# Kernel tuning notes

Hardware: AMD Instinct MI355X
Metric: run time of the kernel (lower is better)

The kernel has to match this reference:

```python
import jax, jax.numpy as jnp
import numpy as np
from itertools import permutations

N_NODES, B, C, H, W = 3, 4, 256, 40, 40
NO_PASS = 2


def _conv3x3(x, w, b):
    # x: [NB, Cin, H, W], w: [Cout, Cin, 3, 3]
    y = jax.lax.conv_general_dilated(
        x, w, window_strides=(1, 1), padding='SAME',
        dimension_numbers=('NCHW', 'OIHW', 'NCHW'))
    return y + b[None, :, None, None]


def setup_inputs() -> dict:
    key = jax.random.key(0)
    ks = jax.random.split(key, 7)
    s = 0.02
    return {
        'nodes': jax.random.normal(ks[0], (N_NODES, B, C, H, W), jnp.float32),
        'theta_w': jax.random.normal(ks[1], (C, C), jnp.float32) * s,
        'theta_b': jax.random.normal(ks[2], (C,), jnp.float32) * s,
        'gru_gates_w': jax.random.normal(ks[3], (2 * C, 2 * C, 3, 3), jnp.float32) * s,
        'gru_gates_b': jax.random.normal(ks[4], (2 * C,), jnp.float32) * s,
        'gru_can_w': jax.random.normal(ks[5], (C, 2 * C, 3, 3), jnp.float32) * s,
        'gru_can_b': jax.random.normal(ks[6], (C,), jnp.float32) * s,
    }


def reference(nodes, theta_w, theta_b, gru_gates_w, gru_gates_b, gru_can_w, gru_can_b):
    N, Bn, Cn, Hn, Wn = nodes.shape
    P = Hn * Wn
    edges = np.array(list(permutations(range(N), 2)))  # [E, 2]
    recv = jnp.asarray(edges[:, 0])  # edge[0] receives message
    send = jnp.asarray(edges[:, 1])  # edge[1] sends

    for _ in range(NO_PASS):
        nf = nodes.reshape(N, Bn, Cn, P)
        # theta is a 1x1 conv == channel matmul
        th = jnp.einsum('oc,nbcp->nbop', theta_w, nf) + theta_b[None, None, :, None]
        thi = th[recv]          # [E, B, C, P]
        ei = nf[recv]           # [E, B, C, P]
        ej = nf[send]           # [E, B, C, P]
        # scores[e,b,p,q] = theta(e1)[:,p] . e2[:,q]
        scores = jnp.einsum('ebcp,ebcq->ebpq', thi, ej)
        atn = jax.nn.softmax(scores, axis=-1)
        # message = atn @ (e2 + e1)^T, back to channel-first
        msg = jnp.einsum('ebpq,ebcq->ebcp', atn, ej + ei)  # [E, B, C, P]
        agg = jax.ops.segment_sum(msg, recv, num_segments=N)  # sum of incoming msgs

        # ConvGRU update, nodes folded into batch dim
        x = agg.reshape(N * Bn, Cn, Hn, Wn)
        h = nodes.reshape(N * Bn, Cn, Hn, Wn)
        gates = _conv3x3(jnp.concatenate([x, h], axis=1), gru_gates_w, gru_gates_b)
        r, z = jnp.split(jax.nn.sigmoid(gates), 2, axis=1)
        cand = jnp.tanh(_conv3x3(jnp.concatenate([x, r * h], axis=1), gru_can_w, gru_can_b))
        h_new = (1.0 - z) * h + z * cand
        nodes = h_new.reshape(N, Bn, Cn, Hn, Wn)
    return nodes
```

## Files before the change

### kernel.cpp

```cpp
#include <hip/hip_runtime.h>
#include <hip/hip_bf16.h>
#include <math.h>

#define NN 3
#define BB 4
#define CC 256
#define C2 512
#define HH 40
#define WW 40
#define PP 1600
#define NBB 12
#define NODESZ (NBB*CC*PP)
#define TO 16
#define PAD 1764

typedef short short8 __attribute__((ext_vector_type(8)));
typedef float f32x4 __attribute__((ext_vector_type(4)));
typedef unsigned short ushort_t;
typedef unsigned int uint_t;

__device__ __forceinline__ ushort_t f2bf(float x) {
  union { float f; uint_t u; } v; v.f = x;
  uint_t r = v.u + 0x7fff + ((v.u >> 16) & 1);
  return (ushort_t)(r >> 16);
}

__device__ __forceinline__ void async_ld16(const ushort_t* g, ushort_t* l) {
  __builtin_amdgcn_global_load_lds(
      (const __attribute__((address_space(1))) uint_t*)g,
      (__attribute__((address_space(3))) uint_t*)l, 16, 0, 0);
}

__global__ void k_copy(const float* __restrict__ in, float* __restrict__ out) {
  int i = blockIdx.x * 256 + threadIdx.x;
  out[i] = in[i];
}

__global__ void k_theta(const float* __restrict__ nodes, const float* __restrict__ tw,
                        const float* __restrict__ tb, ushort_t* __restrict__ th_t) {
  __shared__ float w[TO * CC];
  int t = threadIdx.x;
  int nb = blockIdx.y / (CC / TO);
  int o0 = (blockIdx.y % (CC / TO)) * TO;
  for (int i = t; i < TO * CC; i += 320) w[i] = tw[(o0 + (i >> 8)) * CC + (i & 255)];
  __syncthreads();
  int p = blockIdx.x * 320 + t;
  const float* src = nodes + nb * CC * PP + p;
  float acc[TO];
#pragma unroll
  for (int o = 0; o < TO; ++o) acc[o] = tb[o0 + o];
  for (int c = 0; c < CC; c += 4) {
    float v0 = src[c * PP], v1 = src[(c + 1) * PP], v2 = src[(c + 2) * PP], v3 = src[(c + 3) * PP];
#pragma unroll
    for (int o = 0; o < TO; ++o) {
      const float4 ww = *(const float4*)(w + o * CC + c);
      acc[o] += ww.x * v0 + ww.y * v1 + ww.z * v2 + ww.w * v3;
    }
  }
  size_t base = ((size_t)nb * PP + p) * CC + o0;
#pragma unroll
  for (int o = 0; o < TO; o += 2) {
    uint_t lo = f2bf(acc[o]), hi = f2bf(acc[o + 1]);
    *(uint_t*)&th_t[base + o] = lo | (hi << 16);
  }
}

__global__ void k_to_bf_t(const float* __restrict__ src, ushort_t* __restrict__ dst) {
  __shared__ float tile[32][33];
  int nb = blockIdx.z;
  int c0 = blockIdx.y * 32;
  int pp0 = blockIdx.x * 32;
  int tx = threadIdx.x & 31, ty = threadIdx.x >> 5;
#pragma unroll
  for (int i = 0; i < 4; ++i)
    tile[ty + 8 * i][tx] = src[((size_t)nb * CC + c0 + ty + 8 * i) * PP + pp0 + tx];
  __syncthreads();
#pragma unroll
  for (int i = 0; i < 4; ++i) {
    int q = pp0 + ty + 8 * i;
    int c = c0 + tx;
    int cs = c ^ ((q & 7) << 3);
    dst[((size_t)nb * PP + q) * CC + cs] = f2bf(tile[tx][ty + 8 * i]);
  }
}

__global__ void k_prep_vf(const float* __restrict__ nodes, ushort_t* __restrict__ vf) {
  int T = blockIdx.x;
  int eb = blockIdx.y;
  int e = eb >> 2, b = eb & 3;
  int n = e >> 1, jidx = e & 1;
  int js = jidx + (jidx >= n ? 1 : 0);
  const float* s0 = nodes + (size_t)(n * BB + b) * CC * PP;
  const float* s1 = nodes + (size_t)(js * BB + b) * CC * PP;
  ushort_t* dst = vf + ((size_t)eb * 50 + T) * 8192;
  int t = threadIdx.x;
#pragma unroll
  for (int k = 0; k < 4; ++k) {
    int cid = t + 256 * k;
    int nt = cid >> 6, l = cid & 63;
    int quad = l >> 4, l16 = l & 15;
    int c = 16 * nt + l16;
    int p = 32 * T + quad * 8;
    const float4* a0 = (const float4*)(s0 + (size_t)c * PP + p);
    const float4* a1 = (const float4*)(s1 + (size_t)c * PP + p);
    float4 x0 = a0[0], x1 = a0[1];
    float4 y0 = a1[0], y1 = a1[1];
    short8 o;
    o[0] = (short)f2bf(x0.x + y0.x); o[1] = (short)f2bf(x0.y + y0.y);
    o[2] = (short)f2bf(x0.z + y0.z); o[3] = (short)f2bf(x0.w + y0.w);
    o[4] = (short)f2bf(x1.x + y1.x); o[5] = (short)f2bf(x1.y + y1.y);
    o[6] = (short)f2bf(x1.z + y1.z); o[7] = (short)f2bf(x1.w + y1.w);
    *(short8*)(dst + (size_t)cid * 8) = o;
  }
}

__global__ __launch_bounds__(256, 2) void k_attn_mfma(
    const ushort_t* __restrict__ nodes_bf_t,
    const ushort_t* __restrict__ th_t,
    const ushort_t* __restrict__ vf,
    float* __restrict__ agg_t)
{
  __shared__ ushort_t Ej[32 * 256];
  __shared__ ushort_t Sp[64 * 40];
  __shared__ float Al[64];
  __shared__ float Linv[64];

  const int t = threadIdx.x;
  const int w = t >> 6;
  const int l = t & 63;
  const int quad = l >> 4;
  const int l16 = l & 15;
  const int F = blockIdx.x + 25 * (blockIdx.y + 12 * blockIdx.z);
  const int wk = (F & 7) * 75 + (F >> 3);
  const int p0 = (wk % 25) * 64;
  const int nb = (wk / 25) % 12;
  const int jidx = wk / 300;
  const int n = nb >> 2, b = nb & 3;
  const int e = n * 2 + jidx;
  const int js = jidx + (jidx >= n ? 1 : 0);
  const int eb = e * BB + b;

  const ushort_t* ejb = nodes_bf_t + ((size_t)(js * BB + b) * PP) * CC;
  const ushort_t* vbase = vf + (size_t)eb * 50 * 8192;

  short8 Ath[8];
  {
    const ushort_t* arow = th_t + ((size_t)nb * PP + p0 + 16 * w + l16) * CC + quad * 8;
#pragma unroll
    for (int ks = 0; ks < 8; ++ks) Ath[ks] = *(const short8*)(arow + ks * 32);
  }

  float M = -3.0e38f, Lr = 0.f;
  f32x4 O[4][4];
#pragma unroll
  for (int mt = 0; mt < 4; ++mt)
#pragma unroll
    for (int nt = 0; nt < 4; ++nt)
#pragma unroll
      for (int r = 0; r < 4; ++r) O[mt][nt][r] = 0.f;

#pragma unroll
  for (int i = 0; i < 4; ++i)
    async_ld16(ejb + (4 * w + i) * 512 + l * 8, &Ej[(4 * w + i) * 512]);

  for (int T = 0; T < 50; ++T) {
    __syncthreads();
    short8 Bv[4];
    {
      const ushort_t* vt = vbase + (size_t)T * 8192;
#pragma unroll
      for (int nt = 0; nt < 4; ++nt)
        Bv[nt] = *(const short8*)(vt + (4 * w + nt) * 512 + l * 8);
    }
    f32x4 S0, S1;
#pragma unroll
    for (int r = 0; r < 4; ++r) { S0[r] = 0.f; S1[r] = 0.f; }
#pragma unroll
    for (int ks = 0; ks < 8; ++ks) {
      int ch0 = (((ks * 4 + quad) ^ (l16 & 7)) << 3);
      short8 A0 = *(const short8*)(Ej + l16 * CC + ch0);
      short8 A1 = *(const short8*)(Ej + (16 + l16) * CC + ch0);
      S0 = __builtin_amdgcn_mfma_f32_16x16x32_bf16(A0, Ath[ks], S0, 0, 0, 0);
      S1 = __builtin_amdgcn_mfma_f32_16x16x32_bf16(A1, Ath[ks], S1, 0, 0, 0);
    }
    float m = fmaxf(fmaxf(fmaxf(S0[0], S0[1]), fmaxf(S0[2], S0[3])),
                    fmaxf(fmaxf(S1[0], S1[1]), fmaxf(S1[2], S1[3])));
    m = fmaxf(m, __shfl_xor(m, 16));
    m = fmaxf(m, __shfl_xor(m, 32));
    float Mn = fmaxf(M, m);
    float al = __expf(M - Mn);
    float e0 = __expf(S0[0] - Mn), e1 = __expf(S0[1] - Mn);
    float e2 = __expf(S0[2] - Mn), e3 = __expf(S0[3] - Mn);
    float e4 = __expf(S1[0] - Mn), e5 = __expf(S1[1] - Mn);
    float e6 = __expf(S1[2] - Mn), e7 = __expf(S1[3] - Mn);
    float s = ((e0 + e1) + (e2 + e3)) + ((e4 + e5) + (e6 + e7));
    s += __shfl_xor(s, 16);
    s += __shfl_xor(s, 32);
    Lr = Lr * al + s;
    M = Mn;
    {
      uint2 u;
      u.x = (uint_t)f2bf(e0) | ((uint_t)f2bf(e1) << 16);
      u.y = (uint_t)f2bf(e2) | ((uint_t)f2bf(e3) << 16);
      *(uint2*)&Sp[(16 * w + l16) * 40 + quad * 4] = u;
      uint2 v;
      v.x = (uint_t)f2bf(e4) | ((uint_t)f2bf(e5) << 16);
      v.y = (uint_t)f2bf(e6) | ((uint_t)f2bf(e7) << 16);
      *(uint2*)&Sp[(16 * w + l16) * 40 + 16 + quad * 4] = v;
      if (quad == 0) Al[16 * w + l16] = al;
    }
    __syncthreads();
    if (T < 49) {
#pragma unroll
      for (int i = 0; i < 4; ++i)
        async_ld16(ejb + (size_t)(T + 1) * 8192 + (4 * w + i) * 512 + l * 8,
                   &Ej[(4 * w + i) * 512]);
    }
#pragma unroll
    for (int mt = 0; mt < 4; ++mt) {
      f32x4 a4 = *(const f32x4*)&Al[16 * mt + quad * 4];
#pragma unroll
      for (int nt = 0; nt < 4; ++nt)
#pragma unroll
        for (int r = 0; r < 4; ++r) O[mt][nt][r] *= a4[r];
    }
#pragma unroll
    for (int mt = 0; mt < 4; ++mt) {
      short8 Ap = *(const short8*)&Sp[(16 * mt + l16) * 40 + quad * 8];
#pragma unroll
      for (int nt = 0; nt < 4; ++nt)
        O[mt][nt] = __builtin_amdgcn_mfma_f32_16x16x32_bf16(Ap, Bv[nt], O[mt][nt], 0, 0, 0);
    }
  }
  __syncthreads();
  if (quad == 0) Linv[16 * w + l16] = 1.f / Lr;
  __syncthreads();
  float* ao = agg_t + (((size_t)jidx * NBB + nb) * PP + p0) * CC;
#pragma unroll
  for (int mt = 0; mt < 4; ++mt) {
    f32x4 li = *(const f32x4*)&Linv[16 * mt + quad * 4];
#pragma unroll
    for (int r = 0; r < 4; ++r) {
      float* dst = ao + (size_t)(16 * mt + quad * 4 + r) * CC + 64 * w + l16;
#pragma unroll
      for (int nt = 0; nt < 4; ++nt) dst[16 * nt] = O[mt][nt][r] * li[r];
    }
  }
}


__global__ void k_wrep(const float* __restrict__ w, ushort_t* __restrict__ wr) {
  int i = blockIdx.x * 256 + threadIdx.x;
  int ci = i & 511;
  int rest = i >> 9;
  int tp = rest % 9, co = rest / 9;
  wr[i] = f2bf(w[((size_t)co * 512 + ci) * 9 + tp]);
}

__global__ void k_pad_zero(ushort_t* __restrict__ xpad) {
  int i = blockIdx.x * 256 + threadIdx.x;
  xpad[i] = 0;
}

__global__ void k_pad_agg(const float* __restrict__ agg_t, ushort_t* __restrict__ xpad) {
  int i = blockIdx.x * 256 + threadIdx.x;
  int c = i & 255;
  int rest = i >> 8;
  int px = rest % PP, nb = rest / PP;
  int y = px / 40, x = px - y * 40;
  size_t src = ((size_t)nb * PP + px) * CC + c;
  float v = agg_t[src] + agg_t[(size_t)NBB * PP * CC + src];
  xpad[((size_t)nb * PAD + (y + 1) * 42 + (x + 1)) * C2 + c] = f2bf(v);
}

template <int MODE>
__global__ void k_pad_tr(const float* __restrict__ srcA, const float* __restrict__ srcB,
                         ushort_t* __restrict__ xpad) {
  __shared__ float tile[32][33];
  int nb = blockIdx.z;
  int c0 = blockIdx.y * 32;
  int pp0 = blockIdx.x * 32;
  int tx = threadIdx.x & 31, ty = threadIdx.x >> 5;
#pragma unroll
  for (int i = 0; i < 4; ++i) {
    int c = c0 + ty + 8 * i;
    float v = srcA[((size_t)nb * CC + c) * PP + pp0 + tx];
    if (MODE == 1) v *= srcB[((size_t)nb * C2 + c) * PP + pp0 + tx];
    tile[ty + 8 * i][tx] = v;
  }
  __syncthreads();
#pragma unroll
  for (int i = 0; i < 4; ++i) {
    int px = pp0 + ty + 8 * i;
    int y = px / 40, x = px - y * 40;
    xpad[((size_t)nb * PAD + (y + 1) * 42 + (x + 1)) * C2 + CC + c0 + tx] =
        f2bf(tile[tx][ty + 8 * i]);
  }
}

template <int ACT>
__global__ __launch_bounds__(256) void k_conv_mfma(
    const ushort_t* __restrict__ xpad,
    const ushort_t* __restrict__ wr,
    const float* __restrict__ bias,
    const float* __restrict__ zsrc,
    float* __restrict__ out)
{
  __shared__ ushort_t Asm[2][128 * 32];
  __shared__ ushort_t Bsm[2][128 * 32];
  const int t = threadIdx.x;
  const int w = t >> 6, l = t & 63, quad = l >> 4, l16 = l & 15;
  const int gy = gridDim.y;
  const int F = blockIdx.x + 13 * (blockIdx.y + gy * blockIdx.z);
  const int cpx = (13 * gy * 12) >> 3;
  const int wk = (F & 7) * cpx + (F >> 3);
  const int xw = wk % 13;
  const int rest = wk / 13;
  const int nb = rest % 12;
  const int m0 = (rest / 12) * 128;
  const int px0 = xw * 128;
  const int wm = (w >> 1) * 64, wn = (w & 1) * 64;

  const int lr = l >> 2;
  const int swf = (lr ^ (lr >> 2)) & 3;
  const int lk = ((l & 3) ^ swf) * 8;
  const ushort_t* wsrc = wr + (size_t)(m0 + 32 * w + lr) * 4608 + lk;
  int pxa = px0 + 32 * w + lr;      if (pxa > 1599) pxa = 1599;
  int pxb = pxa + 16;               if (pxb > 1599) pxb = 1599;
  {
    int d = px0 + 32 * w + 16 + lr; if (d <= 1599) pxb = d;
  }
  const int ya = pxa / 40, xa = pxa - ya * 40;
  const int yb = pxb / 40, xb = pxb - yb * 40;
  const ushort_t* bsrc_a = xpad + ((size_t)nb * PAD + ya * 42 + xa) * C2 + lk;
  const ushort_t* bsrc_b = xpad + ((size_t)nb * PAD + yb * 42 + xb) * C2 + lk;

  const int swr = (l16 ^ (l16 >> 2)) & 3;
  const int fk = ((quad ^ swr) * 8);

  f32x4 acc[4][4];
#pragma unroll
  for (int mt = 0; mt < 4; ++mt)
#pragma unroll
    for (int nt = 0; nt < 4; ++nt)
#pragma unroll
      for (int r = 0; r < 4; ++r) acc[mt][nt][r] = 0.f;

  auto stage = [&](int buf, int it) {
    int ci = it / 9;
    int tap = it - ci * 9;
    int cc = ci << 5;
    int ky = tap / 3, kx = tap - ky * 3;
    int boff = (ky * 42 + kx) * C2 + cc;
    const ushort_t* wtap = wsrc + tap * 512 + cc;
    async_ld16(wtap, &Asm[buf][w * 1024]);
    async_ld16(wtap + 16 * 4608, &Asm[buf][w * 1024 + 512]);
    async_ld16(bsrc_a + boff, &Bsm[buf][w * 1024]);
    async_ld16(bsrc_b + boff, &Bsm[buf][w * 1024 + 512]);
  };

  stage(0, 0);
  int cur = 0;
#pragma unroll 1
  for (int it = 0; it < 144; ++it) {
    __syncthreads();
    if (it + 1 < 144) stage(cur ^ 1, it + 1);
    short8 Af[4], Bf[4];
#pragma unroll
    for (int mt = 0; mt < 4; ++mt)
      Af[mt] = *(const short8*)(&Asm[cur][0] + (wm + mt * 16 + l16) * 32 + fk);
#pragma unroll
    for (int nt = 0; nt < 4; ++nt)
      Bf[nt] = *(const short8*)(&Bsm[cur][0] + (wn + nt * 16 + l16) * 32 + fk);
#pragma unroll
    for (int mt = 0; mt < 4; ++mt)
#pragma unroll
      for (int nt = 0; nt < 4; ++nt)
        acc[mt][nt] = __builtin_amdgcn_mfma_f32_16x16x32_bf16(Af[mt], Bf[nt], acc[mt][nt], 0, 0, 0);
    cur ^= 1;
  }

#pragma unroll
  for (int mt = 0; mt < 4; ++mt) {
#pragma unroll
    for (int r = 0; r < 4; ++r) {
      int co = m0 + wm + mt * 16 + quad * 4 + r;
      float bv = bias[co];
#pragma unroll
      for (int nt = 0; nt < 4; ++nt) {
        int px = px0 + wn + nt * 16 + l16;
        if (px >= PP) continue;
        float v = acc[mt][nt][r] + bv;
        if (ACT == 0) {
          out[((size_t)nb * C2 + co) * PP + px] = 1.f / (1.f + __expf(-v));
        } else {
          v = tanhf(v);
          float z = zsrc[((size_t)nb * C2 + CC + co) * PP + px];
          float* hp = out + ((size_t)nb * CC + co) * PP + px;
          float h = *hp;
          *hp = (1.f - z) * h + z * v;
        }
      }
    }
  }
}

extern "C" void kernel_launch(void* const* d_in, const int* in_sizes, int n_in,
                              void* d_out, int out_size, void* d_ws, size_t ws_size,
                              hipStream_t stream) {
  const float* nodes_in = (const float*)d_in[0];
  const float* tw = (const float*)d_in[1];
  const float* tb = (const float*)d_in[2];
  const float* gw = (const float*)d_in[3];
  const float* gb = (const float*)d_in[4];
  const float* cw = (const float*)d_in[5];
  const float* cb = (const float*)d_in[6];

  float* nodes = (float*)d_out;
  char* ws = (char*)d_ws;
  ushort_t* nodes_bf_t = (ushort_t*)ws;
  ushort_t* th_t  = (ushort_t*)(ws + 9830400);
  ushort_t* vf    = (ushort_t*)(ws + 19660800);
  float*    agg_t = (float*)(ws + 39321600);
  ushort_t* xh_pad = (ushort_t*)(ws + 9830400);
  float*    gates = (float*)(ws + 39321600);
  ushort_t* w_g_r = (ushort_t*)(ws + 78643200);
  ushort_t* w_c_r = (ushort_t*)(ws + 83361792);

  k_copy<<<NODESZ / 256, 256, 0, stream>>>(nodes_in, nodes);
  k_wrep<<<(C2 * 9 * C2) / 256, 256, 0, stream>>>(gw, w_g_r);
  k_wrep<<<(CC * 9 * C2) / 256, 256, 0, stream>>>(cw, w_c_r);
  for (int pass = 0; pass < 2; ++pass) {
    k_theta<<<dim3(5, NBB * (CC / TO)), 320, 0, stream>>>(nodes, tw, tb, th_t);
    k_to_bf_t<<<dim3(50, 8, NBB), 256, 0, stream>>>(nodes, nodes_bf_t);
    k_prep_vf<<<dim3(50, 24), 256, 0, stream>>>(nodes, vf);
    k_attn_mfma<<<dim3(25, NBB, 2), 256, 0, stream>>>(nodes_bf_t, th_t, vf, agg_t);
    k_pad_zero<<<(NBB * PAD * C2) / 256, 256, 0, stream>>>(xh_pad);
    k_pad_agg<<<(NBB * PP * CC) / 256, 256, 0, stream>>>(agg_t, xh_pad);
    k_pad_tr<0><<<dim3(50, 8, NBB), 256, 0, stream>>>(nodes, nullptr, xh_pad);
    k_conv_mfma<0><<<dim3(13, 4, NBB), 256, 0, stream>>>(xh_pad, w_g_r, gb, nullptr, gates);
    k_pad_tr<1><<<dim3(50, 8, NBB), 256, 0, stream>>>(nodes, gates, xh_pad);
    k_conv_mfma<1><<<dim3(13, 2, NBB), 256, 0, stream>>>(xh_pad, w_c_r, cb, gates, nodes);
  }
}
```

Measured before the change: 1.079 ms.

## Stage padded input slab once per channel chunk and reuse across all nine taps

The conv implicit-GEMM kernel now loads a contiguous 256-row slab of the padded input into shared memory once per 32-channel chunk. The nine 3x3 taps are then read from that slab at row offsets, instead of re-fetching B tiles from global memory for every tap. This cuts global/L2 traffic for the input operand by roughly the tap count. The cost is double the B shared-memory footprint, per-lane swizzled index arithmetic in the inner loop, and a two-level loop with separate A and B buffer rotation.

```diff
diff --git a/kernel.cpp b/kernel.cpp
--- a/kernel.cpp
+++ b/kernel.cpp
@@ -307,7 +307,7 @@
     float* __restrict__ out)
 {
   __shared__ ushort_t Asm[2][128 * 32];
-  __shared__ ushort_t Bsm[2][128 * 32];
+  __shared__ ushort_t Bsl[2][256 * 32];
   const int t = threadIdx.x;
   const int w = t >> 6, l = t & 63, quad = l >> 4, l16 = l & 15;
   const int gy = gridDim.y;
@@ -325,15 +325,18 @@
   const int swf = (lr ^ (lr >> 2)) & 3;
   const int lk = ((l & 3) ^ swf) * 8;
   const ushort_t* wsrc = wr + (size_t)(m0 + 32 * w + lr) * 4608 + lk;
-  int pxa = px0 + 32 * w + lr;      if (pxa > 1599) pxa = 1599;
-  int pxb = pxa + 16;               if (pxb > 1599) pxb = 1599;
-  {
-    int d = px0 + 32 * w + 16 + lr; if (d <= 1599) pxb = d;
-  }
-  const int ya = pxa / 40, xa = pxa - ya * 40;
-  const int yb = pxb / 40, xb = pxb - yb * 40;
-  const ushort_t* bsrc_a = xpad + ((size_t)nb * PAD + ya * 42 + xa) * C2 + lk;
-  const ushort_t* bsrc_b = xpad + ((size_t)nb * PAD + yb * 42 + xb) * C2 + lk;
+
+  const int slab0 = px0 + 2 * (px0 / 40);
+  const int sgm = ((l >> 2) ^ (l >> 4)) & 3;
+  const ushort_t* bslab_src =
+      xpad + ((size_t)nb * PAD + slab0 + 64 * w + (l >> 2)) * C2 + ((l & 3) ^ sgm) * 8;
+
+  int pb[4];
+#pragma unroll
+  for (int nt = 0; nt < 4; ++nt) {
+    int px = px0 + wn + nt * 16 + l16;
+    pb[nt] = px + 2 * (px / 40) - slab0;
+  }
 
   const int swr = (l16 ^ (l16 >> 2)) & 3;
   const int fk = ((quad ^ swr) * 8);
@@ -346,38 +349,50 @@
 #pragma unroll
       for (int r = 0; r < 4; ++r) acc[mt][nt][r] = 0.f;
 
-  auto stage = [&](int buf, int it) {
+  auto stageA = [&](int buf, int it) {
     int ci = it / 9;
     int tap = it - ci * 9;
-    int cc = ci << 5;
-    int ky = tap / 3, kx = tap - ky * 3;
-    int boff = (ky * 42 + kx) * C2 + cc;
-    const ushort_t* wtap = wsrc + tap * 512 + cc;
-    async_ld16(wtap, &Asm[buf][w * 1024]);
-    async_ld16(wtap + 16 * 4608, &Asm[buf][w * 1024 + 512]);
-    async_ld16(bsrc_a + boff, &Bsm[buf][w * 1024]);
-    async_ld16(bsrc_b + boff, &Bsm[buf][w * 1024 + 512]);
+    const ushort_t* s = wsrc + tap * 512 + ci * 32;
+    async_ld16(s, &Asm[buf][w * 1024]);
+    async_ld16(s + 16 * 4608, &Asm[buf][w * 1024 + 512]);
   };
-
-  stage(0, 0);
-  int cur = 0;
+  auto stageB = [&](int buf, int cc) {
+    const ushort_t* s = bslab_src + cc * 32;
+#pragma unroll
+    for (int i = 0; i < 4; ++i)
+      async_ld16(s + (size_t)i * 16 * C2, &Bsl[buf][w * 2048 + i * 512]);
+  };
+
+  stageB(0, 0);
+  stageA(0, 0);
+  int ab = 0, bb = 0;
 #pragma unroll 1
-  for (int it = 0; it < 144; ++it) {
-    __syncthreads();
-    if (it + 1 < 144) stage(cur ^ 1, it + 1);
-    short8 Af[4], Bf[4];
-#pragma unroll
-    for (int mt = 0; mt < 4; ++mt)
-      Af[mt] = *(const short8*)(&Asm[cur][0] + (wm + mt * 16 + l16) * 32 + fk);
-#pragma unroll
-    for (int nt = 0; nt < 4; ++nt)
-      Bf[nt] = *(const short8*)(&Bsm[cur][0] + (wn + nt * 16 + l16) * 32 + fk);
-#pragma unroll
-    for (int mt = 0; mt < 4; ++mt)
-#pragma unroll
-      for (int nt = 0; nt < 4; ++nt)
-        acc[mt][nt] = __builtin_amdgcn_mfma_f32_16x16x32_bf16(Af[mt], Bf[nt], acc[mt][nt], 0, 0, 0);
-    cur ^= 1;
+  for (int cc = 0; cc < 16; ++cc) {
+#pragma unroll 1
+    for (int tap = 0; tap < 9; ++tap) {
+      __syncthreads();
+      int nit = cc * 9 + tap + 1;
+      if (nit < 144) stageA(ab ^ 1, nit);
+      if (tap == 0 && cc + 1 < 16) stageB(bb ^ 1, cc + 1);
+      const int ky = tap / 3;
+      const int toff = ky * 42 + (tap - 3 * ky);
+      short8 Af[4], Bf[4];
+#pragma unroll
+      for (int mt = 0; mt < 4; ++mt)
+        Af[mt] = *(const short8*)(&Asm[ab][0] + (wm + mt * 16 + l16) * 32 + fk);
+#pragma unroll
+      for (int nt = 0; nt < 4; ++nt) {
+        int R = pb[nt] + toff;
+        Bf[nt] = *(const short8*)(&Bsl[bb][0] + R * 32 + ((quad ^ ((R ^ (R >> 2)) & 3)) << 3));
+      }
+#pragma unroll
+      for (int mt = 0; mt < 4; ++mt)
+#pragma unroll
+        for (int nt = 0; nt < 4; ++nt)
+          acc[mt][nt] = __builtin_amdgcn_mfma_f32_16x16x32_bf16(Af[mt], Bf[nt], acc[mt][nt], 0, 0, 0);
+      ab ^= 1;
+    }
+    bb ^= 1;
   }
 
 #pragma unroll
```

Measured after the change: 1.057 ms. 1.02x faster.
